# Kernel tuning notes

Measured on AMD Instinct MI355X. Metric: run time of the kernel, lower is better.

Reference implementation:

```python
import jax, jax.numpy as jnp
import numpy as np

NUM_HEADS = 16

def setup_inputs() -> dict:
    key = jax.random.key(0)
    k1, k2, k3 = jax.random.split(key, 3)
    B, N, C = 8, 1024, 1024
    x = jax.random.normal(k1, (B, N, C), dtype=jnp.float32)
    qkv_w = jax.random.normal(k2, (3 * C, C), dtype=jnp.float32) * (C ** -0.5)
    proj_w = jax.random.normal(k3, (C, C), dtype=jnp.float32) * (C ** -0.5)
    proj_b = jnp.zeros((C,), dtype=jnp.float32)
    return {"x": x, "qkv_w": qkv_w, "proj_w": proj_w, "proj_b": proj_b}

def reference(x, qkv_w, proj_w, proj_b):
    B, N, C = x.shape
    H = NUM_HEADS
    D = C // H
    scale = D ** -0.5
    qkv = jnp.einsum('bnc,oc->bno', x, qkv_w).reshape(B, N, 3, H, D)
    qkv = jnp.transpose(qkv, (2, 0, 3, 1, 4))
    q, k, v = qkv[0], qkv[1], qkv[2]
    attn = jnp.einsum('bhqd,bhkd->bhqk', q, k) * scale
    attn = jax.nn.softmax(attn, axis=-1)
    out = jnp.einsum('bhqk,bhkd->bhqd', attn, v)
    out = jnp.transpose(out, (0, 2, 1, 3)).reshape(B, N, C)
    out = jnp.einsum('bnc,oc->bno', out, proj_w) + proj_b
    return out
```

## Files before the change

kernel.cpp:

```cpp
#include <hip/hip_runtime.h>
#include <stdint.h>

typedef __attribute__((ext_vector_type(8))) short   short8;
typedef __attribute__((ext_vector_type(4))) float   f32x4;

#define MFMA_16x16x32_BF16 __builtin_amdgcn_mfma_f32_16x16x32_bf16


__device__ inline ushort f2bf(float f) {
  uint32_t u = __builtin_bit_cast(uint32_t, f);
  u = (u + 0x7FFFu + ((u >> 16) & 1u)) >> 16;
  return (ushort)u;
}

__device__ inline void gload16(const void* g, void* l) {
  __builtin_amdgcn_global_load_lds(
      (const __attribute__((address_space(1))) void*)g,
      (__attribute__((address_space(3))) void*)l, 16, 0, 0);
}

__device__ inline int xcd_swz(int bid, int nblk) {
  return (bid & 7) * (nblk >> 3) + (bid >> 3);
}


__global__ __launch_bounds__(256) void cvt3_k(
    const float* __restrict__ a, ushort* __restrict__ oa, int na4,
    const float* __restrict__ b, ushort* __restrict__ ob, int nb4,
    const float* __restrict__ c, ushort* __restrict__ oc, int nc4)
{
  int total = na4 + nb4 + nc4;
  for (int i = blockIdx.x * blockDim.x + threadIdx.x; i < total;
       i += gridDim.x * blockDim.x) {
    const float* in; ushort* out; int j = i;
    if (j < na4)              { in = a; out = oa; }
    else if (j - na4 < nb4)   { in = b; out = ob; j -= na4; }
    else                      { in = c; out = oc; j -= na4 + nb4; }
    float4 v = ((const float4*)in)[j];
    ushort4 o4;
    o4.x = f2bf(v.x); o4.y = f2bf(v.y); o4.z = f2bf(v.z); o4.w = f2bf(v.w);
    ((ushort4*)out)[j] = o4;
  }
}


template<int EPI>
__global__ __launch_bounds__(256, 2) void gemm_bt(
    const ushort* __restrict__ A, const ushort* __restrict__ B,
    int K, int ntm, ushort* __restrict__ outb, float* __restrict__ outf,
    const float* __restrict__ bias)
{
  __shared__ __align__(16) ushort lA[128 * 32];
  __shared__ __align__(16) ushort lB[128 * 32];
  const int nblk = gridDim.x;
  const int l = xcd_swz(blockIdx.x, nblk);
  const int m0 = (l % ntm) * 128;
  const int n0 = (l / ntm) * 128;
  const int tid = threadIdx.x;
  const int lane = tid & 63;
  const int wid  = tid >> 6;
  const int g = lane >> 4, r = lane & 15;
  const int wm = wid >> 1, wn = wid & 1;

  const f32x4 fz = {0.f, 0.f, 0.f, 0.f};
  f32x4 acc[4][4];
  #pragma unroll
  for (int i = 0; i < 4; ++i)
    #pragma unroll
    for (int j = 0; j < 4; ++j) acc[i][j] = fz;

  for (int k0 = 0; k0 < K; k0 += 32) {
    #pragma unroll
    for (int i = 0; i < 2; ++i) {
      int o   = i * 4096 + tid * 16;
      int row = o >> 6;
      int col = (o & 63) >> 1;
      gload16(A + (size_t)(m0 + row) * K + k0 + col, (char*)lA + o);
      gload16(B + (size_t)(n0 + row) * K + k0 + col, (char*)lB + o);
    }
    __syncthreads();

    short8 af[4], bfr[4];
    #pragma unroll
    for (int mi = 0; mi < 4; ++mi)
      af[mi] = *(const short8*)&lA[(wm * 64 + mi * 16 + r) * 32 + g * 8];
    #pragma unroll
    for (int ni = 0; ni < 4; ++ni)
      bfr[ni] = *(const short8*)&lB[(wn * 64 + ni * 16 + r) * 32 + g * 8];
    #pragma unroll
    for (int mi = 0; mi < 4; ++mi)
      #pragma unroll
      for (int ni = 0; ni < 4; ++ni)
        acc[mi][ni] = MFMA_16x16x32_BF16(af[mi], bfr[ni], acc[mi][ni], 0, 0, 0);
    __syncthreads();
  }

  #pragma unroll
  for (int mi = 0; mi < 4; ++mi)
    #pragma unroll
    for (int ni = 0; ni < 4; ++ni)
      #pragma unroll
      for (int reg = 0; reg < 4; ++reg) {
        int rm = m0 + wm * 64 + mi * 16 + g * 4 + reg;
        int cn = n0 + wn * 64 + ni * 16 + r;
        float v = acc[mi][ni][reg];
        if (EPI == 0) {
          int bb = rm >> 10, n = rm & 1023;
          int qi = cn >> 10, rem = cn & 1023;
          size_t base = (size_t)qi * 8388608 + (size_t)bb * 1048576
                      + (size_t)(rem >> 6) * 65536;
          if (qi == 0) v *= 0.18033688011112042f;
          size_t idx = (qi == 2) ? base + (size_t)(rem & 63) * 1024 + n
                                 : base + (size_t)n * 64 + (rem & 63);
          outb[idx] = f2bf(v);
        } else {
          outf[(size_t)rm * 1024 + cn] = v + bias[cn];
        }
      }
}


__device__ inline void stage_k_tile(const ushort* Kg, int kb, ushort* lKb, int tid) {
  #pragma unroll
  for (int i = 0; i < 2; ++i) {
    int o = i * 4096 + tid * 16;
    int krow = o >> 7;
    int scol = ((o & 127) ^ ((krow & 7) << 4)) >> 1;
    gload16(Kg + (size_t)(kb + krow) * 64 + scol, (char*)lKb + o);
  }
}

__device__ inline void stage_v_tile(const ushort* Vtg, int kb, ushort* lVb, int tid) {
  #pragma unroll
  for (int i = 0; i < 2; ++i) {
    int o = i * 4096 + tid * 16;
    int drow = o >> 7;
    int scol = ((o & 127) ^ ((drow & 7) << 4)) >> 1;
    gload16(Vtg + (size_t)drow * 1024 + kb + scol, (char*)lVb + o);
  }
}

__global__ __launch_bounds__(256, 3) void attn_fwd(
    const ushort* __restrict__ qkv, ushort* __restrict__ aout)
{
  __shared__ __align__(16) ushort lK[2][64 * 64];
  __shared__ __align__(16) ushort lV[2][64 * 64];
  __shared__ __align__(16) ushort lP[4 * 16 * 64];
  const int l = xcd_swz(blockIdx.x, 2048);
  const int bh = l >> 4;
  const int b = bh >> 4, h = bh & 15;
  const int tid = threadIdx.x;
  const int lane = tid & 63, wid = tid >> 6;
  const int g = lane >> 4, r = lane & 15;
  const ushort* Qg = qkv + (size_t)bh * 65536;
  const ushort* Kg = qkv + (size_t)(128 + bh) * 65536;
  const ushort* Vg = qkv + (size_t)(256 + bh) * 65536;
  const int q0 = (l & 15) * 64 + wid * 16;

  short8 qf[2];
  #pragma unroll
  for (int c = 0; c < 2; ++c)
    qf[c] = *(const short8*)&Qg[(size_t)(q0 + r) * 64 + c * 32 + g * 8];

  const f32x4 fz = {0.f, 0.f, 0.f, 0.f};
  f32x4 oacc[4] = {fz, fz, fz, fz};
  float lsum[4] = {0.f, 0.f, 0.f, 0.f};

  stage_k_tile(Kg, 0, lK[0], tid);
  stage_v_tile(Vg, 0, lV[0], tid);
  __syncthreads();

  for (int kt = 0; kt < 16; ++kt) {
    const int cur = kt & 1, nxt = cur ^ 1;
    if (kt < 15) {
      stage_k_tile(Kg, (kt + 1) * 64, lK[nxt], tid);
      stage_v_tile(Vg, (kt + 1) * 64, lV[nxt], tid);
    }

    f32x4 s[4] = {fz, fz, fz, fz};
    __builtin_amdgcn_s_setprio(1);
    #pragma unroll
    for (int kf = 0; kf < 4; ++kf)
      #pragma unroll
      for (int c = 0; c < 2; ++c) {
        int row = kf * 16 + r;
        int byt = (row * 128 + (c * 32 + g * 8) * 2) ^ ((row & 7) << 4);
        short8 kfr = *(const short8*)((const char*)lK[cur] + byt);
        s[kf] = MFMA_16x16x32_BF16(qf[c], kfr, s[kf], 0, 0, 0);
      }
    __builtin_amdgcn_s_setprio(0);

    float ps[4][4];
    #pragma unroll
    for (int kf = 0; kf < 4; ++kf)
      #pragma unroll
      for (int reg = 0; reg < 4; ++reg) {
        ps[kf][reg] = exp2f(s[kf][reg]);
        lsum[reg] += ps[kf][reg];
      }
    #pragma unroll
    for (int kf = 0; kf < 4; ++kf)
      #pragma unroll
      for (int rp = 0; rp < 4; rp += 2) {
        uint32_t u;
        asm("v_cvt_pk_bf16_f32 %0, %1, %2" : "=v"(u)
            : "v"(ps[kf][rp]), "v"(ps[kf][rp + 1]));
        int row0 = g * 4 + rp, row1 = row0 + 1, col = kf * 16 + r;
        *(ushort*)((char*)lP + wid * 2048 +
                   ((row0 * 128 + col * 2) ^ ((row0 & 7) << 4))) = (ushort)u;
        *(ushort*)((char*)lP + wid * 2048 +
                   ((row1 * 128 + col * 2) ^ ((row1 & 7) << 4))) = (ushort)(u >> 16);
      }
    asm volatile("s_waitcnt lgkmcnt(0)" ::: "memory");

    short8 pa[2];
    #pragma unroll
    for (int c = 0; c < 2; ++c) {
      int byt = wid * 2048 + ((r * 128 + (c * 32 + g * 8) * 2) ^ ((r & 7) << 4));
      pa[c] = *(const short8*)((const char*)lP + byt);
    }
    __builtin_amdgcn_s_setprio(1);
    #pragma unroll
    for (int n = 0; n < 4; ++n)
      #pragma unroll
      for (int c = 0; c < 2; ++c) {
        int d = n * 16 + r;
        int byt = (d * 128 + (c * 32 + g * 8) * 2) ^ ((d & 7) << 4);
        short8 vb = *(const short8*)((const char*)lV[cur] + byt);
        oacc[n] = MFMA_16x16x32_BF16(pa[c], vb, oacc[n], 0, 0, 0);
      }
    __builtin_amdgcn_s_setprio(0);

    __syncthreads();
  }

  float rl[4];
  #pragma unroll
  for (int reg = 0; reg < 4; ++reg) {
    float su = lsum[reg];
    #pragma unroll
    for (int t = 1; t < 16; t <<= 1) su += __shfl_xor(su, t);
    rl[reg] = 1.0f / su;
  }
  #pragma unroll
  for (int n = 0; n < 4; ++n)
    #pragma unroll
    for (int reg = 0; reg < 4; ++reg) {
      int q = q0 + g * 4 + reg;
      int d = n * 16 + r;
      float v = oacc[n][reg] * rl[reg];
      aout[(size_t)(b * 1024 + q) * 1024 + h * 64 + d] = f2bf(v);
    }
}


extern "C" void kernel_launch(void* const* d_in, const int* in_sizes, int n_in,
                              void* d_out, int out_size, void* d_ws, size_t ws_size,
                              hipStream_t stream)
{
  const float* x      = (const float*)d_in[0];
  const float* qkv_w  = (const float*)d_in[1];
  const float* proj_w = (const float*)d_in[2];
  const float* proj_b = (const float*)d_in[3];
  float* out = (float*)d_out;

  ushort* ws    = (ushort*)d_ws;
  ushort* xb    = ws;
  ushort* wqkv  = xb    + 8388608;
  ushort* wproj = wqkv  + 3145728;
  ushort* qkvb  = wproj + 1048576;
  ushort* attb  = xb;
  if (ws_size < (size_t)37748736 * 2) return;

  cvt3_k<<<2048, 256, 0, stream>>>(x, xb, 8388608 / 4,
                                   qkv_w, wqkv, 3145728 / 4,
                                   proj_w, wproj, 1048576 / 4);

  gemm_bt<0><<<1536, 256, 0, stream>>>(xb,   wqkv,  1024, 64, qkvb, nullptr, nullptr);
  attn_fwd  <<<2048, 256, 0, stream>>>(qkvb, attb);
  gemm_bt<1><<< 512, 256, 0, stream>>>(attb, wproj, 1024, 64, nullptr, out, proj_b);
}
```

Baseline: 292.9 us.

## Double-buffer GEMM LDS tiles with K=64 stages and XOR swizzle

Replaces the single-buffered K=32 GEMM main loop with a double-buffered K=64 loop. The next tile's global-to-LDS loads are issued before the MFMAs on the current tile, and one barrier per iteration is removed. An XOR swizzle on the 16-byte column chunk is applied on both the store and the read side to reduce LDS bank conflicts. LDS use per block grows fourfold (64KB), which may limit occupancy against the 2-blocks launch bound.

```diff
diff --git a/kernel.cpp b/kernel.cpp
--- a/kernel.cpp
+++ b/kernel.cpp
@@ -45,13 +45,29 @@
 
 
 template<int EPI>
+__device__ inline void stage_gemm(const ushort* __restrict__ A,
+                                  const ushort* __restrict__ B,
+                                  int m0, int n0, int K, int k0,
+                                  ushort* lAb, ushort* lBb, int tid)
+{
+  #pragma unroll
+  for (int i = 0; i < 4; ++i) {
+    int o   = i * 4096 + tid * 16;
+    int row = o >> 7;
+    int scol = ((o & 127) ^ ((row & 7) << 4)) >> 1;
+    gload16(A + (size_t)(m0 + row) * K + k0 + scol, (char*)lAb + o);
+    gload16(B + (size_t)(n0 + row) * K + k0 + scol, (char*)lBb + o);
+  }
+}
+
+template<int EPI>
 __global__ __launch_bounds__(256, 2) void gemm_bt(
     const ushort* __restrict__ A, const ushort* __restrict__ B,
     int K, int ntm, ushort* __restrict__ outb, float* __restrict__ outf,
     const float* __restrict__ bias)
 {
-  __shared__ __align__(16) ushort lA[128 * 32];
-  __shared__ __align__(16) ushort lB[128 * 32];
+  __shared__ __align__(16) ushort lA[2][128 * 64];
+  __shared__ __align__(16) ushort lB[2][128 * 64];
   const int nblk = gridDim.x;
   const int l = xcd_swz(blockIdx.x, nblk);
   const int m0 = (l % ntm) * 128;
@@ -69,29 +85,36 @@
     #pragma unroll
     for (int j = 0; j < 4; ++j) acc[i][j] = fz;
 
-  for (int k0 = 0; k0 < K; k0 += 32) {
-    #pragma unroll
-    for (int i = 0; i < 2; ++i) {
-      int o   = i * 4096 + tid * 16;
-      int row = o >> 6;
-      int col = (o & 63) >> 1;
-      gload16(A + (size_t)(m0 + row) * K + k0 + col, (char*)lA + o);
-      gload16(B + (size_t)(n0 + row) * K + k0 + col, (char*)lB + o);
+  const int nkt = K >> 6;
+  stage_gemm<EPI>(A, B, m0, n0, K, 0, lA[0], lB[0], tid);
+  __syncthreads();
+
+  for (int kt = 0; kt < nkt; ++kt) {
+    const int cur = kt & 1;
+    if (kt + 1 < nkt)
+      stage_gemm<EPI>(A, B, m0, n0, K, (kt + 1) * 64, lA[cur ^ 1], lB[cur ^ 1], tid);
+
+    #pragma unroll
+    for (int kk = 0; kk < 2; ++kk) {
+      short8 af[4], bfr[4];
+      #pragma unroll
+      for (int mi = 0; mi < 4; ++mi) {
+        int row = wm * 64 + mi * 16 + r;
+        int byt = row * 128 + (((kk * 4 + g) ^ (r & 7)) << 4);
+        af[mi] = *(const short8*)((const char*)lA[cur] + byt);
+      }
+      #pragma unroll
+      for (int ni = 0; ni < 4; ++ni) {
+        int row = wn * 64 + ni * 16 + r;
+        int byt = row * 128 + (((kk * 4 + g) ^ (r & 7)) << 4);
+        bfr[ni] = *(const short8*)((const char*)lB[cur] + byt);
+      }
+      #pragma unroll
+      for (int mi = 0; mi < 4; ++mi)
+        #pragma unroll
+        for (int ni = 0; ni < 4; ++ni)
+          acc[mi][ni] = MFMA_16x16x32_BF16(af[mi], bfr[ni], acc[mi][ni], 0, 0, 0);
     }
-    __syncthreads();
-
-    short8 af[4], bfr[4];
-    #pragma unroll
-    for (int mi = 0; mi < 4; ++mi)
-      af[mi] = *(const short8*)&lA[(wm * 64 + mi * 16 + r) * 32 + g * 8];
-    #pragma unroll
-    for (int ni = 0; ni < 4; ++ni)
-      bfr[ni] = *(const short8*)&lB[(wn * 64 + ni * 16 + r) * 32 + g * 8];
-    #pragma unroll
-    for (int mi = 0; mi < 4; ++mi)
-      #pragma unroll
-      for (int ni = 0; ni < 4; ++ni)
-        acc[mi][ni] = MFMA_16x16x32_BF16(af[mi], bfr[ni], acc[mi][ni], 0, 0, 0);
     __syncthreads();
   }
 
```

Result: no change. 290.2 us (-0.9%).
